# Kernel optimization log

Measured on AMD Instinct MI355X. Metric: run time of the kernel, lower is better.

## Reference

```python
import jax, jax.numpy as jnp
import numpy as np

ALPHA = 0.1
THETA = 0.5
N_NODES = 50000
N_EDGES = 320000
IN_F, HID, OUT_F, N_LAYERS = 50, 256, 121, 4


def setup_inputs() -> dict:
    key = jax.random.key(0)
    ks = jax.random.split(key, 8)
    x = jax.random.normal(ks[0], (N_NODES, IN_F), dtype=jnp.float32)
    edge_index = jax.random.randint(ks[1], (2, N_EDGES), 0, N_NODES, dtype=jnp.int64)
    edge_weight = jax.random.uniform(ks[2], (N_EDGES,), dtype=jnp.float32) / 8.0  # ~normalized adj values
    lin0_w = jax.random.normal(ks[3], (IN_F, HID), dtype=jnp.float32) / np.sqrt(IN_F)
    lin0_b = jnp.zeros((HID,), dtype=jnp.float32)
    W = jax.random.normal(ks[4], (N_LAYERS, HID, HID), dtype=jnp.float32) / np.sqrt(HID)
    lin1_w = jax.random.normal(ks[5], (HID, OUT_F), dtype=jnp.float32) / np.sqrt(HID)
    lin1_b = jnp.zeros((OUT_F,), dtype=jnp.float32)
    return {"x": x, "edge_index": edge_index, "edge_weight": edge_weight,
            "lin0_w": lin0_w, "lin0_b": lin0_b, "W": W,
            "lin1_w": lin1_w, "lin1_b": lin1_b}


def reference(x, edge_index, edge_weight, lin0_w, lin0_b, W, lin1_w, lin1_b):
    # Eval mode: dropout is identity.
    n = x.shape[0]
    src, dst = edge_index[0], edge_index[1]
    x0 = jax.nn.relu(x @ lin0_w + lin0_b)          # [N, H] initial residual
    h = x0
    for l in range(W.shape[0]):
        beta = jnp.log(THETA / (l + 1) + 1.0)       # GCN2Conv beta, layer = l+1
        # sparse adj propagation: agg[i] = sum_{e: dst=i} w_e * h[src_e]
        agg = jax.ops.segment_sum(edge_weight[:, None] * h[src], dst, num_segments=n)
        s = (1.0 - ALPHA) * agg + ALPHA * x0        # initial-residual mixing
        out = (1.0 - beta) * s + beta * (s @ W[l])  # identity-mapped weight (shared)
        h = jax.nn.relu(out + h)                    # outer residual + relu
    return h @ lin1_w + lin1_b                      # [N, num_classes]
```

## Files before the change

### kernel.cpp

```cpp
#include <hip/hip_runtime.h>
#include <math.h>

#define IN_F   50
#define HID    256
#define OUT_F  121
#define N_LAYERS 4
#define K0PAD  64

typedef __attribute__((ext_vector_type(8))) short short8;
typedef __attribute__((ext_vector_type(4))) float f32x4;

#define GLOBAL_AS __attribute__((address_space(1)))
#define LDS_AS    __attribute__((address_space(3)))

__device__ __forceinline__ ushort f2bf(float f) {
    union { float f; unsigned u; } c; c.f = f;
    unsigned u = c.u;
    u += 0x7fffu + ((u >> 16) & 1u);
    return (ushort)(u >> 16);
}
__device__ __forceinline__ float bf2f(ushort u) {
    union { unsigned u; float f; } c; c.u = ((unsigned)u) << 16;
    return c.f;
}

__global__ void hist_kernel(const int* __restrict__ dst, int* __restrict__ counts, int E) {
    int e = blockIdx.x * blockDim.x + threadIdx.x;
    if (e < E) atomicAdd(&counts[dst[e]], 1);
}

__global__ void scan_phase1(const int* __restrict__ counts, int* __restrict__ row_ptr,
                            int* __restrict__ bsum, int n) {
    __shared__ int sd[1024];
    int t = threadIdx.x;
    int i = blockIdx.x * 1024 + t;
    int v = (i < n) ? counts[i] : 0;
    sd[t] = v;
    __syncthreads();
    for (int off = 1; off < 1024; off <<= 1) {
        int tmp = (t >= off) ? sd[t - off] : 0;
        __syncthreads();
        sd[t] += tmp;
        __syncthreads();
    }
    if (i < n) row_ptr[i] = sd[t] - v;
    if (t == 1023) bsum[blockIdx.x] = sd[1023];
}

__global__ void scan_phase2(int* __restrict__ bsum, int nb) {
    __shared__ int sd[64];
    int t = threadIdx.x;
    int v = (t < nb) ? bsum[t] : 0;
    sd[t] = v;
    __syncthreads();
    for (int off = 1; off < 64; off <<= 1) {
        int tmp = (t >= off) ? sd[t - off] : 0;
        __syncthreads();
        sd[t] += tmp;
        __syncthreads();
    }
    if (t < nb) bsum[t] = sd[t] - v;
    if (t == nb - 1) bsum[nb] = sd[t];
}

__global__ void scan_phase3(int* __restrict__ row_ptr, int* __restrict__ cursor,
                            const int* __restrict__ bsum, int n, int nb) {
    int i = blockIdx.x * 1024 + threadIdx.x;
    if (i < n) {
        int v = row_ptr[i] + bsum[blockIdx.x];
        row_ptr[i] = v;
        cursor[i]  = v;
    }
    if (i == n - 1) row_ptr[n] = bsum[nb];
}

__global__ void scatter_kernel(const int* __restrict__ src, const int* __restrict__ dst,
                               const float* __restrict__ ew, int* __restrict__ cursor,
                               int* __restrict__ col, float* __restrict__ wv, int E) {
    int e = blockIdx.x * blockDim.x + threadIdx.x;
    if (e < E) {
        int d = dst[e];
        int pos = atomicAdd(&cursor[d], 1);
        col[pos] = src[e];
        wv[pos] = ew[e];
    }
}

__global__ void convert_x_kernel(const float* __restrict__ x, ushort* __restrict__ x_bf, int n) {
    int i = blockIdx.x * 256 + threadIdx.x;
    int nd = i >> 6, k = i & 63;
    if (nd < n) x_bf[i] = (k < IN_F) ? f2bf(x[(size_t)nd * IN_F + k]) : 0;
}

__global__ void convert_w0_kernel(const float* __restrict__ w, ushort* __restrict__ wt0) {
    int nn = blockIdx.x;
    int k = threadIdx.x;
    float v = (k < IN_F) ? w[(size_t)k * HID + nn] : 0.f;
    wt0[(size_t)nn * K0PAD + k] = f2bf(v);
}

__global__ void convert_w_kernel(const float* __restrict__ W, ushort* __restrict__ Wt) {
    int nn = blockIdx.x, l = blockIdx.y, k = threadIdx.x;
    float beta = logf(0.5f / (float)(l + 1) + 1.0f);
    float v = beta * W[(size_t)l * HID * HID + (size_t)k * HID + nn];
    if (k == nn) v += 1.0f - beta;
    Wt[(size_t)l * HID * HID + (size_t)nn * HID + k] = f2bf(v);
}

__global__ void convert_w1_kernel(const float* __restrict__ w1, ushort* __restrict__ Wt1) {
    int nn = blockIdx.x;
    int k = threadIdx.x;
    float v = (nn < OUT_F) ? w1[(size_t)k * OUT_F + nn] : 0.f;
    Wt1[(size_t)nn * HID + k] = f2bf(v);
}

__global__ __launch_bounds__(256) void lin0_mfma(
        const ushort* __restrict__ x_bf, const ushort* __restrict__ wt0,
        const float* __restrict__ b, ushort* __restrict__ x0_bf,
        ushort* __restrict__ h_bf, int M) {
    __shared__ ushort As[4][128][8];
    __shared__ ushort Bs[4][128][8];
    int tid = threadIdx.x;
    int wave = tid >> 6;
    int lane = tid & 63;
    int r16 = lane & 15, q = lane >> 4;
    int bm = blockIdx.x * 128;
    int bn = blockIdx.y * 128;
    int wm = (wave >> 1) * 64, wn = (wave & 1) * 64;

    f32x4 acc[4][4] = {};

    int srow = tid & 127;
    int koff0 = tid >> 7;
    int arow = bm + srow; if (arow >= M) arow = M - 1;
    const ushort* aptr = x_bf + (size_t)arow * K0PAD;
    const ushort* bptr = wt0 + (size_t)(bn + srow) * K0PAD;
    char* AsB = (char*)&As[0][0][0];
    char* BsB = (char*)&Bs[0][0][0];
    int woff = wave * 1024;

    const short8* As8 = (const short8*)&As[0][0][0];
    const short8* Bs8 = (const short8*)&Bs[0][0][0];

    for (int k0 = 0; k0 < K0PAD; k0 += 32) {
        __builtin_amdgcn_global_load_lds((const GLOBAL_AS void*)(aptr + k0 + koff0 * 8),
                                         (LDS_AS void*)(AsB + woff), 16, 0, 0);
        __builtin_amdgcn_global_load_lds((const GLOBAL_AS void*)(aptr + k0 + (koff0 + 2) * 8),
                                         (LDS_AS void*)(AsB + 4096 + woff), 16, 0, 0);
        __builtin_amdgcn_global_load_lds((const GLOBAL_AS void*)(bptr + k0 + koff0 * 8),
                                         (LDS_AS void*)(BsB + woff), 16, 0, 0);
        __builtin_amdgcn_global_load_lds((const GLOBAL_AS void*)(bptr + k0 + (koff0 + 2) * 8),
                                         (LDS_AS void*)(BsB + 4096 + woff), 16, 0, 0);
        __syncthreads();

        short8 av[4], bv[4];
#pragma unroll
        for (int mf = 0; mf < 4; ++mf)
            av[mf] = As8[q * 128 + wm + mf * 16 + r16];
#pragma unroll
        for (int nf = 0; nf < 4; ++nf)
            bv[nf] = Bs8[q * 128 + wn + nf * 16 + r16];
#pragma unroll
        for (int mf = 0; mf < 4; ++mf)
#pragma unroll
            for (int nf = 0; nf < 4; ++nf)
                acc[mf][nf] = __builtin_amdgcn_mfma_f32_16x16x32_bf16(av[mf], bv[nf], acc[mf][nf], 0, 0, 0);
        __syncthreads();
    }

#pragma unroll
    for (int mf = 0; mf < 4; ++mf) {
#pragma unroll
        for (int j = 0; j < 4; ++j) {
            int row = bm + wm + mf * 16 + q * 4 + j;
            if (row >= M) continue;
#pragma unroll
            for (int nf = 0; nf < 4; ++nf) {
                int c = bn + wn + nf * 16 + r16;
                size_t idx = (size_t)row * HID + c;
                ushort v = f2bf(fmaxf(acc[mf][nf][j] + b[c], 0.f));
                x0_bf[idx] = v;
                h_bf[idx]  = v;
            }
        }
    }
}

__global__ __launch_bounds__(256) void spmm_mix_kernel(
        const int* __restrict__ row_ptr, const int* __restrict__ col,
        const float* __restrict__ wv, const ushort* __restrict__ h_bf,
        const ushort* __restrict__ x0_bf, ushort* __restrict__ s_bf, int n) {
    int node = (blockIdx.x * 256 + threadIdx.x) >> 6;
    if (node >= n) return;
    int lane = threadIdx.x & 63;
    int f0 = lane * 4;
    int beg = row_ptr[node], end = row_ptr[node + 1];
    float a0 = 0.f, a1 = 0.f, a2 = 0.f, a3 = 0.f;
    int e = beg;
    for (; e + 4 <= end; e += 4) {
        int c0 = col[e], c1 = col[e + 1], c2 = col[e + 2], c3 = col[e + 3];
        float w0 = wv[e], w1 = wv[e + 1], w2 = wv[e + 2], w3 = wv[e + 3];
        ushort4 v0 = *reinterpret_cast<const ushort4*>(&h_bf[(size_t)c0 * HID + f0]);
        ushort4 v1 = *reinterpret_cast<const ushort4*>(&h_bf[(size_t)c1 * HID + f0]);
        ushort4 v2 = *reinterpret_cast<const ushort4*>(&h_bf[(size_t)c2 * HID + f0]);
        ushort4 v3 = *reinterpret_cast<const ushort4*>(&h_bf[(size_t)c3 * HID + f0]);
        a0 = fmaf(w0, bf2f(v0.x), a0); a1 = fmaf(w0, bf2f(v0.y), a1);
        a2 = fmaf(w0, bf2f(v0.z), a2); a3 = fmaf(w0, bf2f(v0.w), a3);
        a0 = fmaf(w1, bf2f(v1.x), a0); a1 = fmaf(w1, bf2f(v1.y), a1);
        a2 = fmaf(w1, bf2f(v1.z), a2); a3 = fmaf(w1, bf2f(v1.w), a3);
        a0 = fmaf(w2, bf2f(v2.x), a0); a1 = fmaf(w2, bf2f(v2.y), a1);
        a2 = fmaf(w2, bf2f(v2.z), a2); a3 = fmaf(w2, bf2f(v2.w), a3);
        a0 = fmaf(w3, bf2f(v3.x), a0); a1 = fmaf(w3, bf2f(v3.y), a1);
        a2 = fmaf(w3, bf2f(v3.z), a2); a3 = fmaf(w3, bf2f(v3.w), a3);
    }
    if (e + 2 <= end) {
        int c0 = col[e], c1 = col[e + 1];
        float w0 = wv[e], w1 = wv[e + 1];
        ushort4 v0 = *reinterpret_cast<const ushort4*>(&h_bf[(size_t)c0 * HID + f0]);
        ushort4 v1 = *reinterpret_cast<const ushort4*>(&h_bf[(size_t)c1 * HID + f0]);
        a0 = fmaf(w0, bf2f(v0.x), a0); a1 = fmaf(w0, bf2f(v0.y), a1);
        a2 = fmaf(w0, bf2f(v0.z), a2); a3 = fmaf(w0, bf2f(v0.w), a3);
        a0 = fmaf(w1, bf2f(v1.x), a0); a1 = fmaf(w1, bf2f(v1.y), a1);
        a2 = fmaf(w1, bf2f(v1.z), a2); a3 = fmaf(w1, bf2f(v1.w), a3);
        e += 2;
    }
    if (e < end) {
        int c0 = col[e];
        float w0 = wv[e];
        ushort4 v0 = *reinterpret_cast<const ushort4*>(&h_bf[(size_t)c0 * HID + f0]);
        a0 = fmaf(w0, bf2f(v0.x), a0); a1 = fmaf(w0, bf2f(v0.y), a1);
        a2 = fmaf(w0, bf2f(v0.z), a2); a3 = fmaf(w0, bf2f(v0.w), a3);
    }
    size_t idx = (size_t)node * HID + f0;
    ushort4 xv = *reinterpret_cast<const ushort4*>(&x0_bf[idx]);
    ushort4 r;
    r.x = f2bf(0.9f * a0 + 0.1f * bf2f(xv.x));
    r.y = f2bf(0.9f * a1 + 0.1f * bf2f(xv.y));
    r.z = f2bf(0.9f * a2 + 0.1f * bf2f(xv.z));
    r.w = f2bf(0.9f * a3 + 0.1f * bf2f(xv.w));
    *reinterpret_cast<ushort4*>(&s_bf[idx]) = r;
}

__global__ __launch_bounds__(256) void gemm_mfma_layer(
        const ushort* __restrict__ s_bf, const ushort* __restrict__ wt,
        ushort* __restrict__ h_bf, int M) {
    __shared__ ushort As[4][128][8];
    __shared__ ushort Bs[4][128][8];
    int tid = threadIdx.x;
    int wave = tid >> 6;
    int lane = tid & 63;
    int r16 = lane & 15, q = lane >> 4;
    int bm = blockIdx.x * 128;
    int bn = blockIdx.y * 128;
    int wm = (wave >> 1) * 64, wn = (wave & 1) * 64;

    f32x4 acc[4][4] = {};

    int srow = tid & 127;
    int koff0 = tid >> 7;
    int arow = bm + srow; if (arow >= M) arow = M - 1;
    const ushort* aptr = s_bf + (size_t)arow * HID;
    const ushort* bptr = wt + (size_t)(bn + srow) * HID;
    char* AsB = (char*)&As[0][0][0];
    char* BsB = (char*)&Bs[0][0][0];
    int woff = wave * 1024;

    const short8* As8 = (const short8*)&As[0][0][0];
    const short8* Bs8 = (const short8*)&Bs[0][0][0];

    for (int k0 = 0; k0 < HID; k0 += 32) {
        __builtin_amdgcn_global_load_lds((const GLOBAL_AS void*)(aptr + k0 + koff0 * 8),
                                         (LDS_AS void*)(AsB + woff), 16, 0, 0);
        __builtin_amdgcn_global_load_lds((const GLOBAL_AS void*)(aptr + k0 + (koff0 + 2) * 8),
                                         (LDS_AS void*)(AsB + 4096 + woff), 16, 0, 0);
        __builtin_amdgcn_global_load_lds((const GLOBAL_AS void*)(bptr + k0 + koff0 * 8),
                                         (LDS_AS void*)(BsB + woff), 16, 0, 0);
        __builtin_amdgcn_global_load_lds((const GLOBAL_AS void*)(bptr + k0 + (koff0 + 2) * 8),
                                         (LDS_AS void*)(BsB + 4096 + woff), 16, 0, 0);
        __syncthreads();

        short8 av[4], bv[4];
#pragma unroll
        for (int mf = 0; mf < 4; ++mf)
            av[mf] = As8[q * 128 + wm + mf * 16 + r16];
#pragma unroll
        for (int nf = 0; nf < 4; ++nf)
            bv[nf] = Bs8[q * 128 + wn + nf * 16 + r16];
#pragma unroll
        for (int mf = 0; mf < 4; ++mf)
#pragma unroll
            for (int nf = 0; nf < 4; ++nf)
                acc[mf][nf] = __builtin_amdgcn_mfma_f32_16x16x32_bf16(av[mf], bv[nf], acc[mf][nf], 0, 0, 0);
        __syncthreads();
    }

#pragma unroll
    for (int mf = 0; mf < 4; ++mf) {
#pragma unroll
        for (int j = 0; j < 4; ++j) {
            int row = bm + wm + mf * 16 + q * 4 + j;
            if (row >= M) continue;
#pragma unroll
            for (int nf = 0; nf < 4; ++nf) {
                int c = bn + wn + nf * 16 + r16;
                size_t idx = (size_t)row * HID + c;
                float v = fmaxf(acc[mf][nf][j] + bf2f(h_bf[idx]), 0.f);
                h_bf[idx] = f2bf(v);
            }
        }
    }
}

__global__ __launch_bounds__(256) void lin1_mfma(
        const ushort* __restrict__ h_bf, const ushort* __restrict__ wt1,
        const float* __restrict__ b, float* __restrict__ out, int M) {
    __shared__ ushort As[4][128][8];
    __shared__ ushort Bs[4][128][8];
    int tid = threadIdx.x;
    int wave = tid >> 6;
    int lane = tid & 63;
    int r16 = lane & 15, q = lane >> 4;
    int bm = blockIdx.x * 128;
    int wm = (wave >> 1) * 64, wn = (wave & 1) * 64;

    f32x4 acc[4][4] = {};

    int srow = tid & 127;
    int koff0 = tid >> 7;
    int arow = bm + srow; if (arow >= M) arow = M - 1;
    const ushort* aptr = h_bf + (size_t)arow * HID;
    const ushort* bptr = wt1 + (size_t)srow * HID;
    char* AsB = (char*)&As[0][0][0];
    char* BsB = (char*)&Bs[0][0][0];
    int woff = wave * 1024;

    const short8* As8 = (const short8*)&As[0][0][0];
    const short8* Bs8 = (const short8*)&Bs[0][0][0];

    for (int k0 = 0; k0 < HID; k0 += 32) {
        __builtin_amdgcn_global_load_lds((const GLOBAL_AS void*)(aptr + k0 + koff0 * 8),
                                         (LDS_AS void*)(AsB + woff), 16, 0, 0);
        __builtin_amdgcn_global_load_lds((const GLOBAL_AS void*)(aptr + k0 + (koff0 + 2) * 8),
                                         (LDS_AS void*)(AsB + 4096 + woff), 16, 0, 0);
        __builtin_amdgcn_global_load_lds((const GLOBAL_AS void*)(bptr + k0 + koff0 * 8),
                                         (LDS_AS void*)(BsB + woff), 16, 0, 0);
        __builtin_amdgcn_global_load_lds((const GLOBAL_AS void*)(bptr + k0 + (koff0 + 2) * 8),
                                         (LDS_AS void*)(BsB + 4096 + woff), 16, 0, 0);
        __syncthreads();

        short8 av[4], bv[4];
#pragma unroll
        for (int mf = 0; mf < 4; ++mf)
            av[mf] = As8[q * 128 + wm + mf * 16 + r16];
#pragma unroll
        for (int nf = 0; nf < 4; ++nf)
            bv[nf] = Bs8[q * 128 + wn + nf * 16 + r16];
#pragma unroll
        for (int mf = 0; mf < 4; ++mf)
#pragma unroll
            for (int nf = 0; nf < 4; ++nf)
                acc[mf][nf] = __builtin_amdgcn_mfma_f32_16x16x32_bf16(av[mf], bv[nf], acc[mf][nf], 0, 0, 0);
        __syncthreads();
    }

#pragma unroll
    for (int mf = 0; mf < 4; ++mf) {
#pragma unroll
        for (int j = 0; j < 4; ++j) {
            int row = bm + wm + mf * 16 + q * 4 + j;
            if (row >= M) continue;
#pragma unroll
            for (int nf = 0; nf < 4; ++nf) {
                int c = wn + nf * 16 + r16;
                if (c < OUT_F)
                    out[(size_t)row * OUT_F + c] = acc[mf][nf][j] + b[c];
            }
        }
    }
}

extern "C" void kernel_launch(void* const* d_in, const int* in_sizes, int n_in,
                              void* d_out, int out_size, void* d_ws, size_t ws_size,
                              hipStream_t stream) {
    const float* x      = (const float*)d_in[0];
    const int*   ei     = (const int*)d_in[1];
    const float* ew     = (const float*)d_in[2];
    const float* lin0_w = (const float*)d_in[3];
    const float* lin0_b = (const float*)d_in[4];
    const float* W      = (const float*)d_in[5];
    const float* lin1_w = (const float*)d_in[6];
    const float* lin1_b = (const float*)d_in[7];
    float* out = (float*)d_out;

    int N = in_sizes[0] / IN_F;
    int E = in_sizes[2];
    const int* src = ei;
    const int* dst = ei + E;

    char* ws = (char*)d_ws;
    ushort* x0_bf   = (ushort*)ws; ws += (size_t)N * HID * 2;
    ushort* h_bf    = (ushort*)ws; ws += (size_t)N * HID * 2;
    ushort* s_bf    = (ushort*)ws; ws += (size_t)N * HID * 2;
    ushort* x_bf    = (ushort*)ws; ws += (size_t)N * K0PAD * 2;
    ushort* Wt0     = (ushort*)ws; ws += (size_t)HID * K0PAD * 2;
    ushort* Wt      = (ushort*)ws; ws += (size_t)N_LAYERS * HID * HID * 2;
    ushort* Wt1     = (ushort*)ws; ws += (size_t)128 * HID * 2;
    int*    row_ptr = (int*)ws;    ws += (size_t)(N + 1) * 4;
    int*    counts  = (int*)ws;    ws += (size_t)N * 4;
    int*    cursor  = (int*)ws;    ws += (size_t)N * 4;
    int*    bsum    = (int*)ws;    ws += (size_t)128 * 4;
    int*    col     = (int*)ws;    ws += (size_t)E * 4;
    float*  wv      = (float*)ws;  ws += (size_t)E * 4;

    int nb = (N + 1023) / 1024;

    hipMemsetAsync(counts, 0, (size_t)N * 4, stream);
    hist_kernel<<<(E + 255) / 256, 256, 0, stream>>>(dst, counts, E);
    scan_phase1<<<nb, 1024, 0, stream>>>(counts, row_ptr, bsum, N);
    scan_phase2<<<1, 64, 0, stream>>>(bsum, nb);
    scan_phase3<<<nb, 1024, 0, stream>>>(row_ptr, cursor, bsum, N, nb);
    scatter_kernel<<<(E + 255) / 256, 256, 0, stream>>>(src, dst, ew, cursor, col, wv, E);

    convert_x_kernel<<<(N * K0PAD + 255) / 256, 256, 0, stream>>>(x, x_bf, N);
    convert_w0_kernel<<<HID, K0PAD, 0, stream>>>(lin0_w, Wt0);
    convert_w_kernel<<<dim3(HID, N_LAYERS), HID, 0, stream>>>(W, Wt);
    convert_w1_kernel<<<128, HID, 0, stream>>>(lin1_w, Wt1);

    int mblocks = (N + 127) / 128;
    lin0_mfma<<<dim3(mblocks, 2), 256, 0, stream>>>(x_bf, Wt0, lin0_b, x0_bf, h_bf, N);

    for (int l = 0; l < N_LAYERS; ++l) {
        spmm_mix_kernel<<<(N + 3) / 4, 256, 0, stream>>>(row_ptr, col, wv, h_bf, x0_bf, s_bf, N);
        gemm_mfma_layer<<<dim3(mblocks, 2), 256, 0, stream>>>(
            s_bf, Wt + (size_t)l * HID * HID, h_bf, N);
    }

    lin1_mfma<<<mblocks, 256, 0, stream>>>(h_bf, Wt1, lin1_b, out, N);
}
```

Baseline: 352.4 us.

## Fuse SpMM aggregation into per-layer GEMM via LDS tile; merge prep kernels

Each layer's sparse aggregation and residual mix is now computed directly into a swizzled 128x256 LDS tile. The same block then runs the full-width MFMA GEMM on that tile, which removes the s_bf round trip through global memory and one launch per layer. h is ping-ponged between two buffers, since rows from other blocks are read as neighbours. All conversion kernels and the counts memset are merged into one prep kernel. The cost is 64KB+ of LDS per block with only 391 blocks, so occupancy and latency hiding for the irregular gather may drop.

```diff
diff --git a/kernel.cpp b/kernel.cpp
--- a/kernel.cpp
+++ b/kernel.cpp
@@ -22,6 +22,46 @@
 __device__ __forceinline__ float bf2f(ushort u) {
     union { unsigned u; float f; } c; c.u = ((unsigned)u) << 16;
     return c.f;
+}
+
+__global__ __launch_bounds__(256) void prep_kernel(
+        const float* __restrict__ x, const float* __restrict__ w0,
+        const float* __restrict__ W, const float* __restrict__ w1,
+        ushort* __restrict__ x_bf, ushort* __restrict__ wt0,
+        ushort* __restrict__ Wt, ushort* __restrict__ wt1,
+        int* __restrict__ counts, int n) {
+    long long flat = (long long)blockIdx.x * 256 + threadIdx.x;
+    long long r0 = (long long)n * K0PAD;
+    if (flat < r0) {
+        int nd = (int)(flat >> 6), k = (int)(flat & 63);
+        x_bf[flat] = (k < IN_F) ? f2bf(x[(size_t)nd * IN_F + k]) : 0;
+        return;
+    }
+    flat -= r0;
+    if (flat < HID * K0PAD) {
+        int nn = (int)(flat >> 6), k = (int)(flat & 63);
+        wt0[flat] = (k < IN_F) ? f2bf(w0[(size_t)k * HID + nn]) : 0;
+        return;
+    }
+    flat -= HID * K0PAD;
+    if (flat < N_LAYERS * HID * HID) {
+        int l = (int)(flat >> 16);
+        int rem = (int)(flat & 65535);
+        int nn = rem >> 8, k = rem & 255;
+        float beta = logf(0.5f / (float)(l + 1) + 1.0f);
+        float v = beta * W[(size_t)l * HID * HID + (size_t)k * HID + nn];
+        if (k == nn) v += 1.0f - beta;
+        Wt[flat] = f2bf(v);
+        return;
+    }
+    flat -= N_LAYERS * HID * HID;
+    if (flat < 128 * HID) {
+        int nn = (int)(flat >> 8), k = (int)(flat & 255);
+        wt1[flat] = (nn < OUT_F) ? f2bf(w1[(size_t)k * OUT_F + nn]) : 0;
+        return;
+    }
+    flat -= 128 * HID;
+    if (flat < n) counts[flat] = 0;
 }
 
 __global__ void hist_kernel(const int* __restrict__ dst, int* __restrict__ counts, int E) {
@@ -84,34 +124,6 @@
         col[pos] = src[e];
         wv[pos] = ew[e];
     }
-}
-
-__global__ void convert_x_kernel(const float* __restrict__ x, ushort* __restrict__ x_bf, int n) {
-    int i = blockIdx.x * 256 + threadIdx.x;
-    int nd = i >> 6, k = i & 63;
-    if (nd < n) x_bf[i] = (k < IN_F) ? f2bf(x[(size_t)nd * IN_F + k]) : 0;
-}
-
-__global__ void convert_w0_kernel(const float* __restrict__ w, ushort* __restrict__ wt0) {
-    int nn = blockIdx.x;
-    int k = threadIdx.x;
-    float v = (k < IN_F) ? w[(size_t)k * HID + nn] : 0.f;
-    wt0[(size_t)nn * K0PAD + k] = f2bf(v);
-}
-
-__global__ void convert_w_kernel(const float* __restrict__ W, ushort* __restrict__ Wt) {
-    int nn = blockIdx.x, l = blockIdx.y, k = threadIdx.x;
-    float beta = logf(0.5f / (float)(l + 1) + 1.0f);
-    float v = beta * W[(size_t)l * HID * HID + (size_t)k * HID + nn];
-    if (k == nn) v += 1.0f - beta;
-    Wt[(size_t)l * HID * HID + (size_t)nn * HID + k] = f2bf(v);
-}
-
-__global__ void convert_w1_kernel(const float* __restrict__ w1, ushort* __restrict__ Wt1) {
-    int nn = blockIdx.x;
-    int k = threadIdx.x;
-    float v = (nn < OUT_F) ? w1[(size_t)k * OUT_F + nn] : 0.f;
-    Wt1[(size_t)nn * HID + k] = f2bf(v);
 }
 
 __global__ __launch_bounds__(256) void lin0_mfma(
@@ -186,106 +198,96 @@
     }
 }
 
-__global__ __launch_bounds__(256) void spmm_mix_kernel(
+__global__ __launch_bounds__(512) void layer_fused(
         const int* __restrict__ row_ptr, const int* __restrict__ col,
-        const float* __restrict__ wv, const ushort* __restrict__ h_bf,
-        const ushort* __restrict__ x0_bf, ushort* __restrict__ s_bf, int n) {
-    int node = (blockIdx.x * 256 + threadIdx.x) >> 6;
-    if (node >= n) return;
-    int lane = threadIdx.x & 63;
-    int f0 = lane * 4;
-    int beg = row_ptr[node], end = row_ptr[node + 1];
-    float a0 = 0.f, a1 = 0.f, a2 = 0.f, a3 = 0.f;
-    int e = beg;
-    for (; e + 4 <= end; e += 4) {
-        int c0 = col[e], c1 = col[e + 1], c2 = col[e + 2], c3 = col[e + 3];
-        float w0 = wv[e], w1 = wv[e + 1], w2 = wv[e + 2], w3 = wv[e + 3];
-        ushort4 v0 = *reinterpret_cast<const ushort4*>(&h_bf[(size_t)c0 * HID + f0]);
-        ushort4 v1 = *reinterpret_cast<const ushort4*>(&h_bf[(size_t)c1 * HID + f0]);
-        ushort4 v2 = *reinterpret_cast<const ushort4*>(&h_bf[(size_t)c2 * HID + f0]);
-        ushort4 v3 = *reinterpret_cast<const ushort4*>(&h_bf[(size_t)c3 * HID + f0]);
-        a0 = fmaf(w0, bf2f(v0.x), a0); a1 = fmaf(w0, bf2f(v0.y), a1);
-        a2 = fmaf(w0, bf2f(v0.z), a2); a3 = fmaf(w0, bf2f(v0.w), a3);
-        a0 = fmaf(w1, bf2f(v1.x), a0); a1 = fmaf(w1, bf2f(v1.y), a1);
-        a2 = fmaf(w1, bf2f(v1.z), a2); a3 = fmaf(w1, bf2f(v1.w), a3);
-        a0 = fmaf(w2, bf2f(v2.x), a0); a1 = fmaf(w2, bf2f(v2.y), a1);
-        a2 = fmaf(w2, bf2f(v2.z), a2); a3 = fmaf(w2, bf2f(v2.w), a3);
-        a0 = fmaf(w3, bf2f(v3.x), a0); a1 = fmaf(w3, bf2f(v3.y), a1);
-        a2 = fmaf(w3, bf2f(v3.z), a2); a3 = fmaf(w3, bf2f(v3.w), a3);
-    }
-    if (e + 2 <= end) {
-        int c0 = col[e], c1 = col[e + 1];
-        float w0 = wv[e], w1 = wv[e + 1];
-        ushort4 v0 = *reinterpret_cast<const ushort4*>(&h_bf[(size_t)c0 * HID + f0]);
-        ushort4 v1 = *reinterpret_cast<const ushort4*>(&h_bf[(size_t)c1 * HID + f0]);
-        a0 = fmaf(w0, bf2f(v0.x), a0); a1 = fmaf(w0, bf2f(v0.y), a1);
-        a2 = fmaf(w0, bf2f(v0.z), a2); a3 = fmaf(w0, bf2f(v0.w), a3);
-        a0 = fmaf(w1, bf2f(v1.x), a0); a1 = fmaf(w1, bf2f(v1.y), a1);
-        a2 = fmaf(w1, bf2f(v1.z), a2); a3 = fmaf(w1, bf2f(v1.w), a3);
-        e += 2;
-    }
-    if (e < end) {
-        int c0 = col[e];
-        float w0 = wv[e];
-        ushort4 v0 = *reinterpret_cast<const ushort4*>(&h_bf[(size_t)c0 * HID + f0]);
-        a0 = fmaf(w0, bf2f(v0.x), a0); a1 = fmaf(w0, bf2f(v0.y), a1);
-        a2 = fmaf(w0, bf2f(v0.z), a2); a3 = fmaf(w0, bf2f(v0.w), a3);
-    }
-    size_t idx = (size_t)node * HID + f0;
-    ushort4 xv = *reinterpret_cast<const ushort4*>(&x0_bf[idx]);
-    ushort4 r;
-    r.x = f2bf(0.9f * a0 + 0.1f * bf2f(xv.x));
-    r.y = f2bf(0.9f * a1 + 0.1f * bf2f(xv.y));
-    r.z = f2bf(0.9f * a2 + 0.1f * bf2f(xv.z));
-    r.w = f2bf(0.9f * a3 + 0.1f * bf2f(xv.w));
-    *reinterpret_cast<ushort4*>(&s_bf[idx]) = r;
-}
-
-__global__ __launch_bounds__(256) void gemm_mfma_layer(
-        const ushort* __restrict__ s_bf, const ushort* __restrict__ wt,
-        ushort* __restrict__ h_bf, int M) {
-    __shared__ ushort As[4][128][8];
-    __shared__ ushort Bs[4][128][8];
+        const float* __restrict__ wv, const ushort* __restrict__ h_in,
+        const ushort* __restrict__ x0_bf, const ushort* __restrict__ wt,
+        ushort* __restrict__ h_out, int n) {
+    __shared__ ushort s_tile[128 * 256];
+    __shared__ ushort Bs[4 * 256 * 8];
     int tid = threadIdx.x;
     int wave = tid >> 6;
     int lane = tid & 63;
+    int bm = blockIdx.x * 128;
+
+    {
+        int f0 = lane * 4;
+        int kb = lane * 8;
+        for (int i = 0; i < 16; ++i) {
+            int r = wave * 16 + i;
+            int node = bm + r;
+            ushort4 res;
+            if (node < n) {
+                float a0 = 0.f, a1 = 0.f, a2 = 0.f, a3 = 0.f;
+                int beg = row_ptr[node], end = row_ptr[node + 1];
+                int e = beg;
+                for (; e + 4 <= end; e += 4) {
+                    int c0 = col[e], c1 = col[e + 1], c2 = col[e + 2], c3 = col[e + 3];
+                    float w0 = wv[e], w1 = wv[e + 1], w2 = wv[e + 2], w3 = wv[e + 3];
+                    ushort4 v0 = *reinterpret_cast<const ushort4*>(&h_in[(size_t)c0 * HID + f0]);
+                    ushort4 v1 = *reinterpret_cast<const ushort4*>(&h_in[(size_t)c1 * HID + f0]);
+                    ushort4 v2 = *reinterpret_cast<const ushort4*>(&h_in[(size_t)c2 * HID + f0]);
+                    ushort4 v3 = *reinterpret_cast<const ushort4*>(&h_in[(size_t)c3 * HID + f0]);
+                    a0 = fmaf(w0, bf2f(v0.x), a0); a1 = fmaf(w0, bf2f(v0.y), a1);
+                    a2 = fmaf(w0, bf2f(v0.z), a2); a3 = fmaf(w0, bf2f(v0.w), a3);
+                    a0 = fmaf(w1, bf2f(v1.x), a0); a1 = fmaf(w1, bf2f(v1.y), a1);
+                    a2 = fmaf(w1, bf2f(v1.z), a2); a3 = fmaf(w1, bf2f(v1.w), a3);
+                    a0 = fmaf(w2, bf2f(v2.x), a0); a1 = fmaf(w2, bf2f(v2.y), a1);
+                    a2 = fmaf(w2, bf2f(v2.z), a2); a3 = fmaf(w2, bf2f(v2.w), a3);
+                    a0 = fmaf(w3, bf2f(v3.x), a0); a1 = fmaf(w3, bf2f(v3.y), a1);
+                    a2 = fmaf(w3, bf2f(v3.z), a2); a3 = fmaf(w3, bf2f(v3.w), a3);
+                }
+                for (; e < end; ++e) {
+                    int c0 = col[e];
+                    float w0 = wv[e];
+                    ushort4 v0 = *reinterpret_cast<const ushort4*>(&h_in[(size_t)c0 * HID + f0]);
+                    a0 = fmaf(w0, bf2f(v0.x), a0); a1 = fmaf(w0, bf2f(v0.y), a1);
+                    a2 = fmaf(w0, bf2f(v0.z), a2); a3 = fmaf(w0, bf2f(v0.w), a3);
+                }
+                size_t idx = (size_t)node * HID + f0;
+                ushort4 xv = *reinterpret_cast<const ushort4*>(&x0_bf[idx]);
+                res.x = f2bf(0.9f * a0 + 0.1f * bf2f(xv.x));
+                res.y = f2bf(0.9f * a1 + 0.1f * bf2f(xv.y));
+                res.z = f2bf(0.9f * a2 + 0.1f * bf2f(xv.z));
+                res.w = f2bf(0.9f * a3 + 0.1f * bf2f(xv.w));
+            } else {
+                res.x = 0; res.y = 0; res.z = 0; res.w = 0;
+            }
+            *reinterpret_cast<ushort4*>((char*)s_tile + r * 512 + (kb ^ ((r & 7) << 4))) = res;
+        }
+    }
+    __syncthreads();
+
     int r16 = lane & 15, q = lane >> 4;
-    int bm = blockIdx.x * 128;
-    int bn = blockIdx.y * 128;
-    int wm = (wave >> 1) * 64, wn = (wave & 1) * 64;
-
+    int wm = (wave >> 2) * 64, wn = (wave & 3) * 64;
     f32x4 acc[4][4] = {};
-
-    int srow = tid & 127;
-    int koff0 = tid >> 7;
-    int arow = bm + srow; if (arow >= M) arow = M - 1;
-    const ushort* aptr = s_bf + (size_t)arow * HID;
-    const ushort* bptr = wt + (size_t)(bn + srow) * HID;
-    char* AsB = (char*)&As[0][0][0];
-    char* BsB = (char*)&Bs[0][0][0];
-    int woff = wave * 1024;
-
-    const short8* As8 = (const short8*)&As[0][0][0];
-    const short8* Bs8 = (const short8*)&Bs[0][0][0];
+    char* BsB = (char*)Bs;
+    const short8* Bs8 = (const short8*)Bs;
 
     for (int k0 = 0; k0 < HID; k0 += 32) {
-        __builtin_amdgcn_global_load_lds((const GLOBAL_AS void*)(aptr + k0 + koff0 * 8),
-                                         (LDS_AS void*)(AsB + woff), 16, 0, 0);
-        __builtin_amdgcn_global_load_lds((const GLOBAL_AS void*)(aptr + k0 + (koff0 + 2) * 8),
-                                         (LDS_AS void*)(AsB + 4096 + woff), 16, 0, 0);
-        __builtin_amdgcn_global_load_lds((const GLOBAL_AS void*)(bptr + k0 + koff0 * 8),
-                                         (LDS_AS void*)(BsB + woff), 16, 0, 0);
-        __builtin_amdgcn_global_load_lds((const GLOBAL_AS void*)(bptr + k0 + (koff0 + 2) * 8),
-                                         (LDS_AS void*)(BsB + 4096 + woff), 16, 0, 0);
+        {
+            int nn0 = tid & 255, kc0 = tid >> 8;
+            __builtin_amdgcn_global_load_lds(
+                (const GLOBAL_AS void*)(wt + (size_t)nn0 * HID + k0 + kc0 * 8),
+                (LDS_AS void*)(BsB + tid * 16), 16, 0, 0);
+            int flat1 = tid + 512;
+            int nn1 = flat1 & 255, kc1 = flat1 >> 8;
+            __builtin_amdgcn_global_load_lds(
+                (const GLOBAL_AS void*)(wt + (size_t)nn1 * HID + k0 + kc1 * 8),
+                (LDS_AS void*)(BsB + flat1 * 16), 16, 0, 0);
+        }
         __syncthreads();
 
         short8 av[4], bv[4];
 #pragma unroll
-        for (int mf = 0; mf < 4; ++mf)
-            av[mf] = As8[q * 128 + wm + mf * 16 + r16];
+        for (int mf = 0; mf < 4; ++mf) {
+            int row = wm + mf * 16 + r16;
+            int kbyte = (2 * k0 + q * 16) ^ ((row & 7) << 4);
+            av[mf] = *reinterpret_cast<const short8*>((const char*)s_tile + row * 512 + kbyte);
+        }
 #pragma unroll
         for (int nf = 0; nf < 4; ++nf)
-            bv[nf] = Bs8[q * 128 + wn + nf * 16 + r16];
+            bv[nf] = Bs8[q * 256 + wn + nf * 16 + r16];
 #pragma unroll
         for (int mf = 0; mf < 4; ++mf)
 #pragma unroll
@@ -299,13 +301,13 @@
 #pragma unroll
         for (int j = 0; j < 4; ++j) {
             int row = bm + wm + mf * 16 + q * 4 + j;
-            if (row >= M) continue;
+            if (row >= n) continue;
 #pragma unroll
             for (int nf = 0; nf < 4; ++nf) {
-                int c = bn + wn + nf * 16 + r16;
+                int c = wn + nf * 16 + r16;
                 size_t idx = (size_t)row * HID + c;
-                float v = fmaxf(acc[mf][nf][j] + bf2f(h_bf[idx]), 0.f);
-                h_bf[idx] = f2bf(v);
+                float v = fmaxf(acc[mf][nf][j] + bf2f(h_in[idx]), 0.f);
+                h_out[idx] = f2bf(v);
             }
         }
     }
@@ -399,8 +401,8 @@
 
     char* ws = (char*)d_ws;
     ushort* x0_bf   = (ushort*)ws; ws += (size_t)N * HID * 2;
-    ushort* h_bf    = (ushort*)ws; ws += (size_t)N * HID * 2;
-    ushort* s_bf    = (ushort*)ws; ws += (size_t)N * HID * 2;
+    ushort* h_a     = (ushort*)ws; ws += (size_t)N * HID * 2;
+    ushort* h_b     = (ushort*)ws; ws += (size_t)N * HID * 2;
     ushort* x_bf    = (ushort*)ws; ws += (size_t)N * K0PAD * 2;
     ushort* Wt0     = (ushort*)ws; ws += (size_t)HID * K0PAD * 2;
     ushort* Wt      = (ushort*)ws; ws += (size_t)N_LAYERS * HID * HID * 2;
@@ -414,26 +416,26 @@
 
     int nb = (N + 1023) / 1024;
 
-    hipMemsetAsync(counts, 0, (size_t)N * 4, stream);
+    size_t prep_tot = (size_t)N * K0PAD + HID * K0PAD
+                    + (size_t)N_LAYERS * HID * HID + 128 * HID + N;
+    prep_kernel<<<(int)((prep_tot + 255) / 256), 256, 0, stream>>>(
+        x, lin0_w, W, lin1_w, x_bf, Wt0, Wt, Wt1, counts, N);
+
     hist_kernel<<<(E + 255) / 256, 256, 0, stream>>>(dst, counts, E);
     scan_phase1<<<nb, 1024, 0, stream>>>(counts, row_ptr, bsum, N);
     scan_phase2<<<1, 64, 0, stream>>>(bsum, nb);
     scan_phase3<<<nb, 1024, 0, stream>>>(row_ptr, cursor, bsum, N, nb);
     scatter_kernel<<<(E + 255) / 256, 256, 0, stream>>>(src, dst, ew, cursor, col, wv, E);
 
-    convert_x_kernel<<<(N * K0PAD + 255) / 256, 256, 0, stream>>>(x, x_bf, N);
-    convert_w0_kernel<<<HID, K0PAD, 0, stream>>>(lin0_w, Wt0);
-    convert_w_kernel<<<dim3(HID, N_LAYERS), HID, 0, stream>>>(W, Wt);
-    convert_w1_kernel<<<128, HID, 0, stream>>>(lin1_w, Wt1);
-
     int mblocks = (N + 127) / 128;
-    lin0_mfma<<<dim3(mblocks, 2), 256, 0, stream>>>(x_bf, Wt0, lin0_b, x0_bf, h_bf, N);
+    lin0_mfma<<<dim3(mblocks, 2), 256, 0, stream>>>(x_bf, Wt0, lin0_b, x0_bf, h_a, N);
 
     for (int l = 0; l < N_LAYERS; ++l) {
-        spmm_mix_kernel<<<(N + 3) / 4, 256, 0, stream>>>(row_ptr, col, wv, h_bf, x0_bf, s_bf, N);
-        gemm_mfma_layer<<<dim3(mblocks, 2), 256, 0, stream>>>(
-            s_bf, Wt + (size_t)l * HID * HID, h_bf, N);
-    }
-
-    lin1_mfma<<<mblocks, 256, 0, stream>>>(h_bf, Wt1, lin1_b, out, N);
-}
+        const ushort* hin  = (l & 1) ? h_b : h_a;
+        ushort*       hout = (l & 1) ? h_a : h_b;
+        layer_fused<<<mblocks, 512, 0, stream>>>(
+            row_ptr, col, wv, hin, x0_bf, Wt + (size_t)l * HID * HID, hout, N);
+    }
+
+    lin1_mfma<<<mblocks, 256, 0, stream>>>(h_a, Wt1, lin1_b, out, N);
+}
```

Result: slower. 368.4 us (+4.5%).
